# Kernel tuning notes

Measured on AMD Instinct MI355X. Metric: run time of the kernel, lower is better.

The kernel has to match this reference:

```python
import jax, jax.numpy as jnp
import numpy as np

NUM_BINS = 36
EPS = 1e-12
BASE_DROP, MIN_DROP, MAX_DROP = 0.3, 0.1, 0.6
SENSITIVITY, NORMAL_APE = 4.0, 0.78


def _hann(n):
    # torch.hann_window default (periodic=True): 0.5*(1 - cos(2*pi*k/N))
    return 0.5 - 0.5 * jnp.cos(2.0 * jnp.pi * jnp.arange(n, dtype=jnp.float32) / n)


def compute_ape(images):
    B, C, H, W = images.shape
    mean = jnp.array([0.485, 0.456, 0.406], dtype=images.dtype).reshape(1, 3, 1, 1)
    std = jnp.array([0.229, 0.224, 0.225], dtype=images.dtype).reshape(1, 3, 1, 1)
    wts = jnp.array([0.2989, 0.587, 0.114], dtype=images.dtype).reshape(1, 3, 1, 1)
    gray = ((images * std + mean) * wts).sum(axis=1)  # (B,H,W)
    gray = gray - gray.mean(axis=(1, 2), keepdims=True)
    gray = gray * (_hann(H)[:, None] * _hann(W)[None, :])
    P = jnp.abs(jnp.fft.fft2(gray)) ** 2
    P = jnp.fft.fftshift(P, axes=(1, 2))
    cy, cx = (H - 1) / 2.0, (W - 1) / 2.0
    yy = jnp.arange(H, dtype=jnp.float32)[:, None] - cy
    xx = jnp.arange(W, dtype=jnp.float32)[None, :] - cx
    r = jnp.sqrt(xx ** 2 + yy ** 2)
    theta = (jnp.arctan2(yy, xx) + 2 * jnp.pi) % (2 * jnp.pi)
    r_max = r.max()
    radial_mask = (r >= 0.05 * r_max) & (r <= 0.95 * r_max)
    bin_width = 2 * jnp.pi / NUM_BINS
    idx = jnp.clip((theta / bin_width).astype(jnp.int32), 0, NUM_BINS - 1)  # (H,W)
    # batched masked angular histogram: one segment_sum over B*NUM_BINS segments
    Pm = (P * radial_mask).reshape(B, -1)
    seg = (idx.reshape(-1)[None, :] + NUM_BINS * jnp.arange(B)[:, None]).reshape(-1)
    energy = jax.ops.segment_sum(Pm.reshape(-1), seg, num_segments=B * NUM_BINS)
    energy = energy.reshape(B, NUM_BINS)
    total = energy.sum(axis=1, keepdims=True)
    p = energy / (total + EPS)
    H_theta = -(p * jnp.log(p + EPS)).sum(axis=1)
    ape = jnp.clip(H_theta / np.log(NUM_BINS), 0.0, 1.0)
    return jnp.where(total[:, 0] <= EPS, 0.0, ape)


def ape_to_dropout_prob(ape):
    adj = jnp.tanh((NORMAL_APE - ape) * SENSITIVITY)
    drop = jnp.where(adj >= 0,
                     BASE_DROP + adj * (MAX_DROP - BASE_DROP),
                     BASE_DROP + adj * (BASE_DROP - MIN_DROP))
    return jnp.clip(drop, MIN_DROP, MAX_DROP)


def adaptive_dropout(x, probs, key):
    # per-sample dropout: mask ~ Bernoulli(1-p), scale by 1/(1-p+1e-8)
    p = probs[:, None, None]
    keep = jax.random.bernoulli(key, 1.0 - p, x.shape).astype(x.dtype)
    out = x * keep / (1.0 - p + 1e-8)
    return jnp.where(p > 0, out, x)


def setup_inputs() -> dict:
    key = jax.random.key(0)
    k1, k2, k3, k4 = jax.random.split(key, 4)
    B, N, D, Hf = 64, 256, 768, 768
    images = jax.random.uniform(k1, (B, 3, 448, 448), dtype=jnp.float32)
    x = jax.random.normal(k2, (B, N, D), dtype=jnp.float32)
    w1 = jax.random.normal(k3, (Hf, D), dtype=jnp.float32) * (1.0 / np.sqrt(D))
    w2 = jax.random.normal(k4, (D, Hf), dtype=jnp.float32) * (1.0 / np.sqrt(Hf))
    return {"images": images, "x": x, "w1": w1, "w2": w2}


def reference(images, x, w1, w2):
    ape = compute_ape(images)
    probs = jax.lax.stop_gradient(ape_to_dropout_prob(ape))  # torch casts to python float -> detached
    k0, k1, k2 = jax.random.split(jax.random.key(1), 3)
    h = adaptive_dropout(x, probs, k0)            # input dropout
    h = jnp.einsum('bnd,hd->bnh', h, w1)          # fc1 (bias=False)
    h = jax.nn.gelu(h, approximate=False)         # nn.GELU (exact erf)
    h = adaptive_dropout(h, probs, k1)
    y = jnp.einsum('bnh,dh->bnd', h, w2)          # fc2 (bias=False)
    y = adaptive_dropout(y, probs, k2)
    return y
```

## Files before the change

kernel.cpp:

```cpp
#include <hip/hip_runtime.h>
#include <stdint.h>
#include <math.h>

typedef __attribute__((ext_vector_type(8))) short short8;
typedef __attribute__((ext_vector_type(4))) float floatx4;

#define IMGN 448
#define HW   200704
#define NBATCH 64
#define NBINS 36

#define MFMA(a, b, c) __builtin_amdgcn_mfma_f32_16x16x32_bf16((a), (b), (c), 0, 0, 0)

#define WAITBAR6() asm volatile("s_waitcnt vmcnt(6)\ns_barrier" ::: "memory")
#define WAITBAR0() asm volatile("s_waitcnt vmcnt(0)\ns_barrier" ::: "memory")
#define ENDBAR()   asm volatile("s_waitcnt lgkmcnt(0)\ns_barrier" ::: "memory")

#define WS_WIN   0u
#define WS_BINS  4096u
#define WS_TS    24576u
#define WS_BIDX  32768u
#define WS_TW    1048576u
#define TWSZ     401408u
#define WS_W     4194304u
#define WSZ      1179648u
#define WS_REG1  16777216u
#define GSZ      25690112u
#define CBSZ     13762560u
#define XSZ      25165824u
#define WS_REG2  75497472u

__host__ __device__ __forceinline__ uint32_t rotl32(uint32_t v, int r) {
  return (v << r) | (v >> (32 - r));
}
__host__ __device__ __forceinline__ void tf2x32(uint32_t k0, uint32_t k1,
                                                uint32_t x0, uint32_t x1,
                                                uint32_t &o0, uint32_t &o1) {
  uint32_t k2 = k0 ^ k1 ^ 0x1BD11BDAu;
  uint32_t v0 = x0 + k0, v1 = x1 + k1;
#define TFR(r) { v0 += v1; v1 = rotl32(v1, r); v1 ^= v0; }
  TFR(13) TFR(15) TFR(26) TFR(6)   v0 += k1; v1 += k2 + 1u;
  TFR(17) TFR(29) TFR(16) TFR(24)  v0 += k2; v1 += k0 + 2u;
  TFR(13) TFR(15) TFR(26) TFR(6)   v0 += k0; v1 += k1 + 3u;
  TFR(17) TFR(29) TFR(16) TFR(24)  v0 += k1; v1 += k2 + 4u;
  TFR(13) TFR(15) TFR(26) TFR(6)   v0 += k2; v1 += k0 + 5u;
#undef TFR
  o0 = v0; o1 = v1;
}
__device__ __forceinline__ float tf_uniform(uint32_t k0, uint32_t k1, uint32_t idx) {
  uint32_t a, b;
  tf2x32(k0, k1, 0u, idx, a, b);
  uint32_t bits = a ^ b;
  return __uint_as_float((bits >> 9) | 0x3F800000u) - 1.0f;
}

__device__ __forceinline__ unsigned short bf16rne(float v) {
  unsigned u = __float_as_uint(v);
  return (unsigned short)((u + 0x7fffu + ((u >> 16) & 1u)) >> 16);
}
__device__ __forceinline__ void split2(float v, unsigned short &h, unsigned short &l) {
  h = bf16rne(v);
  float fh = __uint_as_float(((unsigned)h) << 16);
  l = bf16rne(v - fh);
}

__device__ __forceinline__ float fast_erf(float x) {
  float ax = fabsf(x);
  float t = 1.0f / (1.0f + 0.3275911f * ax);
  float p = t * (0.254829592f + t * (-0.284496736f + t * (1.421413741f +
            t * (-1.453152027f + t * 1.061405429f))));
  float y = 1.0f - p * __expf(-ax * ax);
  return __uint_as_float((__float_as_uint(y) & 0x7fffffffu) |
                         (__float_as_uint(x) & 0x80000000u));
}

__device__ __forceinline__ void gload16(const void *g, void *l) {
  __builtin_amdgcn_global_load_lds(
      (const __attribute__((address_space(1))) unsigned int *)g,
      (__attribute__((address_space(3))) unsigned int *)l, 16, 0, 0);
}

__global__ __launch_bounds__(256) void k_prep(float *__restrict__ win,
                                              double *__restrict__ bins,
                                              uint8_t *__restrict__ bidx) {
  int t = blockIdx.x * 256 + threadIdx.x;
  int a = t / IMGN, b = t % IMGN;
  double yy = (double)((a + 224) % IMGN) - 223.5;
  double xx = (double)((b + 224) % IMGN) - 223.5;
  double r2 = xx * xx + yy * yy;
  uint8_t idx = 255;
  if (r2 >= 249.76125 && r2 <= 90163.81125) {
    double th = atan2(yy, xx);
    if (th < 0.0) th += 6.283185307179586476925286766559;
    int i = (int)(th / 0.17453292519943295769236907684886);
    if (i > 35) i = 35;
    if (i < 0) i = 0;
    idx = (uint8_t)i;
  }
  bidx[t] = idx;
  if (t < IMGN) {
    double ang = 6.283185307179586476925286766559 * (double)t / 448.0;
    win[t] = (float)(0.5 - 0.5 * cos(ang));
  }
  if (t < NBATCH * NBINS) bins[t] = 0.0;
}

__global__ __launch_bounds__(256) void k_tw(short8 *__restrict__ tch, short8 *__restrict__ tcl,
                                            short8 *__restrict__ tsh, short8 *__restrict__ tsl) {
  int wid = blockIdx.x * 256 + threadIdx.x;
  int lane = wid & 63;
  int tmp = wid >> 6;
  int kb = tmp % 14, mb = tmp / 14;
  int m = mb * 16 + (lane & 15);
  int k0 = kb * 32 + (lane >> 4) * 8;
  short8 ch, cl, sh, sl;
#pragma unroll
  for (int e = 0; e < 8; ++e) {
    int mm = (m * (k0 + e)) % IMGN;
    double ang = -6.283185307179586476925286766559 * (double)mm / 448.0;
    float c = (float)cos(ang), s = (float)sin(ang);
    unsigned short h, l;
    split2(c, h, l); ch[e] = (short)h; cl[e] = (short)l;
    split2(s, h, l); sh[e] = (short)h; sl[e] = (short)l;
  }
  tch[wid] = ch; tcl[wid] = cl; tsh[wid] = sh; tsl[wid] = sl;
}

__global__ __launch_bounds__(256) void k_wconv(const float *__restrict__ w1, const float *__restrict__ w2,
                                               short8 *__restrict__ w1h, short8 *__restrict__ w1l,
                                               short8 *__restrict__ w2h, short8 *__restrict__ w2l) {
  int wid = blockIdx.x * 256 + threadIdx.x;
  const float *src = blockIdx.y ? w2 : w1;
  short8 *dh = blockIdx.y ? w2h : w1h;
  short8 *dl = blockIdx.y ? w2l : w1l;
  int lane = wid & 63;
  int tmp = wid >> 6;
  int kb = tmp % 24, nb = tmp / 24;
  int n = nb * 16 + (lane & 15);
  int k0 = kb * 32 + (lane >> 4) * 8;
  const float *p = src + (size_t)n * 768 + k0;
  short8 vh, vl;
#pragma unroll
  for (int e = 0; e < 8; ++e) {
    unsigned short h, l;
    split2(p[e], h, l);
    vh[e] = (short)h; vl[e] = (short)l;
  }
  dh[wid] = vh; dl[wid] = vl;
}

__global__ __launch_bounds__(256) void k_gprep(const float *__restrict__ img, const float *__restrict__ win,
                                               short8 *__restrict__ gh, short8 *__restrict__ gl) {
  int wid = blockIdx.x * 256 + threadIdx.x;
  int lane = wid & 63;
  int tmp = wid >> 6;
  int kb = tmp % 14, nb = tmp / 14;
  int n = nb * 16 + (lane & 15);
  int b = n / 448, y = n % 448;
  int x0 = kb * 32 + (lane >> 4) * 8;
  const float *p = img + (size_t)b * 3 * HW + y * IMGN + x0;
  float wy = win[y];
  short8 vh, vl;
#pragma unroll
  for (int e = 0; e < 8; ++e) {
    float r = p[e], g = p[HW + e], bl = p[2 * HW + e];
    float t0 = (r * 0.229f + 0.485f) * 0.2989f;
    float t1 = (g * 0.224f + 0.456f) * 0.587f;
    float t2 = (bl * 0.225f + 0.406f) * 0.114f;
    float v = ((t0 + t1) + t2) * wy * win[x0 + e];
    unsigned short h, l;
    split2(v, h, l);
    vh[e] = (short)h; vl[e] = (short)l;
  }
  gh[wid] = vh; gl[wid] = vl;
}

__global__ __launch_bounds__(256) void k_rows(const short8 *__restrict__ tch, const short8 *__restrict__ tcl,
                                              const short8 *__restrict__ tsh, const short8 *__restrict__ tsl,
                                              const short8 *__restrict__ gh, const short8 *__restrict__ gl,
                                              short8 *__restrict__ crh, short8 *__restrict__ crl,
                                              short8 *__restrict__ cih, short8 *__restrict__ cil) {
  __shared__ short8 S[512];
  int orig = blockIdx.x;
  int swz = (orig & 7) * 224 + (orig >> 3);
  int mtg = swz & 3, ntg = swz >> 2;
  int tid = threadIdx.x;
  int lane = tid & 63, w = tid >> 6;
  int g = lane >> 4, c = lane & 15;
  int mt = mtg * 4 + w;
  floatx4 s_c[4] = {}, s_s[4] = {};
  for (int kb = 0; kb < 14; ++kb) {
#pragma unroll
    for (int i = 0; i < 2; ++i) {
      int ch = w * 2 + i;
      const short8 *m0 = (ch >> 2) ? gl : gh;
      int row = ntg * 4 + (ch & 3);
      gload16(m0 + ((size_t)row * 14 + kb) * 64 + lane, (char *)S + ch * 1024);
    }
    int ao = (mt * 14 + kb) * 64 + lane;
    short8 ach = tch[ao], acl = tcl[ao], ash = tsh[ao], asl = tsl[ao];
    __syncthreads();
#pragma unroll
    for (int nt = 0; nt < 4; ++nt) {
      short8 bh = S[nt * 64 + lane];
      short8 bl = S[(4 + nt) * 64 + lane];
      s_c[nt] = MFMA(ach, bh, s_c[nt]);
      s_c[nt] = MFMA(ach, bl, s_c[nt]);
      s_c[nt] = MFMA(acl, bh, s_c[nt]);
      s_s[nt] = MFMA(ash, bh, s_s[nt]);
      s_s[nt] = MFMA(ash, bl, s_s[nt]);
      s_s[nt] = MFMA(asl, bh, s_s[nt]);
    }
    __syncthreads();
  }
#pragma unroll
  for (int nt = 0; nt < 4; ++nt) {
    int nrow = (ntg * 4 + nt) * 16 + c;
    int b = nrow / 448, y = nrow % 448;
    int kb2 = y >> 5;
    int lofs = 16 * ((y & 31) >> 3);
    int e2 = y & 7;
#pragma unroll
    for (int r = 0; r < 4; ++r) {
      int v = mt * 16 + 4 * g + r;
      if (v < 240) {
        int n2 = b * 240 + v;
        size_t word = ((size_t)(n2 >> 4) * 14 + kb2) * 64 + (n2 & 15) + lofs;
        unsigned short h, l;
        split2(s_c[nt][r], h, l);
        ((unsigned short *)crh)[word * 8 + e2] = h;
        ((unsigned short *)crl)[word * 8 + e2] = l;
        split2(s_s[nt][r], h, l);
        ((unsigned short *)cih)[word * 8 + e2] = h;
        ((unsigned short *)cil)[word * 8 + e2] = l;
      }
    }
  }
}

__global__ __launch_bounds__(128) void k_cols(const short8 *__restrict__ tch, const short8 *__restrict__ tcl,
                                              const short8 *__restrict__ tsh, const short8 *__restrict__ tsl,
                                              const short8 *__restrict__ crh, const short8 *__restrict__ crl,
                                              const short8 *__restrict__ cih, const short8 *__restrict__ cil,
                                              const uint8_t *__restrict__ bidx, double *__restrict__ bins) {
  __shared__ short8 S[1024];
  __shared__ double lb[72];
  int orig = blockIdx.x;
  int swz = (orig & 7) * 210 + (orig >> 3);
  int mtg = swz % 7, ntg = swz / 7;
  int tid = threadIdx.x;
  if (tid < 72) lb[tid] = 0.0;
  int lane = tid & 63, w = tid >> 6;
  int g = lane >> 4, c = lane & 15;
  int mt0 = mtg * 4 + w * 2;
  int nt0 = ntg * 4;
  floatx4 cc0[4] = {}, sc0[4] = {}, ss0[4] = {}, cs0[4] = {};
  floatx4 cc1[4] = {}, sc1[4] = {}, ss1[4] = {}, cs1[4] = {};
  for (int kb = 0; kb < 14; ++kb) {
#pragma unroll
    for (int i = 0; i < 8; ++i) {
      int ch = w * 8 + i;
      int sel = ch >> 2;
      const short8 *m0 = sel == 0 ? crh : sel == 1 ? crl : sel == 2 ? cih : cil;
      int row = nt0 + (ch & 3);
      gload16(m0 + ((size_t)row * 14 + kb) * 64 + lane, (char *)S + ch * 1024);
    }
    int ao = (mt0 * 14 + kb) * 64 + lane;
    short8 c0 = tch[ao], l0 = tcl[ao], s0 = tsh[ao], z0 = tsl[ao];
    short8 c1 = tch[ao + 896], l1 = tcl[ao + 896], s1 = tsh[ao + 896], z1 = tsl[ao + 896];
    __syncthreads();
#pragma unroll
    for (int nt = 0; nt < 4; ++nt) {
      short8 brh = S[nt * 64 + lane];
      short8 brl = S[(4 + nt) * 64 + lane];
      short8 bih = S[(8 + nt) * 64 + lane];
      short8 bil = S[(12 + nt) * 64 + lane];
      cc0[nt] = MFMA(c0, brh, cc0[nt]);
      cc0[nt] = MFMA(c0, brl, cc0[nt]);
      cc0[nt] = MFMA(l0, brh, cc0[nt]);
      sc0[nt] = MFMA(s0, brh, sc0[nt]);
      sc0[nt] = MFMA(s0, brl, sc0[nt]);
      sc0[nt] = MFMA(z0, brh, sc0[nt]);
      ss0[nt] = MFMA(s0, bih, ss0[nt]);
      ss0[nt] = MFMA(s0, bil, ss0[nt]);
      ss0[nt] = MFMA(z0, bih, ss0[nt]);
      cs0[nt] = MFMA(c0, bih, cs0[nt]);
      cs0[nt] = MFMA(c0, bil, cs0[nt]);
      cs0[nt] = MFMA(l0, bih, cs0[nt]);
      cc1[nt] = MFMA(c1, brh, cc1[nt]);
      cc1[nt] = MFMA(c1, brl, cc1[nt]);
      cc1[nt] = MFMA(l1, brh, cc1[nt]);
      sc1[nt] = MFMA(s1, brh, sc1[nt]);
      sc1[nt] = MFMA(s1, brl, sc1[nt]);
      sc1[nt] = MFMA(z1, brh, sc1[nt]);
      ss1[nt] = MFMA(s1, bih, ss1[nt]);
      ss1[nt] = MFMA(s1, bil, ss1[nt]);
      ss1[nt] = MFMA(z1, bih, ss1[nt]);
      cs1[nt] = MFMA(c1, bih, cs1[nt]);
      cs1[nt] = MFMA(c1, bil, cs1[nt]);
      cs1[nt] = MFMA(l1, bih, cs1[nt]);
    }
    __syncthreads();
  }
  int base_b = (ntg * 64) / 240;
  int cb0 = -1, cb1 = -1, cb2 = -1, cb3 = -1;
  double cv0 = 0.0, cv1 = 0.0, cv2 = 0.0, cv3 = 0.0;
#define PUTBIN(slot_, val_)                                                    \
  { int _s = (slot_); double _v = (val_);                                      \
    if (_s == cb0) cv0 += _v;                                                  \
    else if (_s == cb1) cv1 += _v;                                             \
    else if (_s == cb2) cv2 += _v;                                             \
    else if (_s == cb3) cv3 += _v;                                             \
    else {                                                                     \
      if (cb3 >= 0) atomicAdd(&lb[cb3], cv3);                                  \
      cb3 = cb2; cv3 = cv2; cb2 = cb1; cv2 = cv1;                              \
      cb1 = cb0; cv1 = cv0; cb0 = _s; cv0 = _v;                                \
    } }
#define C_EPI(CC, SC, SS, CS, MT)                                              \
  {                                                                            \
    _Pragma("unroll") for (int nt = 0; nt < 4; ++nt) {                         \
      int n = (nt0 + nt) * 16 + c;                                             \
      int v = n % 240;                                                         \
      int bloc = n / 240 - base_b;                                             \
      if (v < 225) {                                                           \
        _Pragma("unroll") for (int r = 0; r < 4; ++r) {                        \
          int u = (MT) * 16 + 4 * g + r;                                       \
          float frv = CC[nt][r] - SS[nt][r];                                   \
          float fiv = SC[nt][r] + CS[nt][r];                                   \
          double P = (double)frv * frv + (double)fiv * fiv;                    \
          int i1 = bidx[u * IMGN + v];                                         \
          if (i1 < 36) PUTBIN(bloc * 36 + i1, P);                              \
          if (v >= 1 && v <= 223) {                                            \
            int i2 = bidx[((IMGN - u) % IMGN) * IMGN + (IMGN - v)];            \
            if (i2 < 36) PUTBIN(bloc * 36 + i2, P);                            \
          }                                                                    \
        }                                                                      \
      }                                                                        \
    }                                                                          \
  }
  C_EPI(cc0, sc0, ss0, cs0, mt0)
  C_EPI(cc1, sc1, ss1, cs1, mt0 + 1)
#undef C_EPI
  if (cb0 >= 0) atomicAdd(&lb[cb0], cv0);
  if (cb1 >= 0) atomicAdd(&lb[cb1], cv1);
  if (cb2 >= 0) atomicAdd(&lb[cb2], cv2);
  if (cb3 >= 0) atomicAdd(&lb[cb3], cv3);
#undef PUTBIN
  __syncthreads();
  if (tid < 72) {
    int bb = base_b + tid / 36;
    if (bb < NBATCH && lb[tid] != 0.0) atomicAdd(&bins[bb * NBINS + (tid % 36)], lb[tid]);
  }
}

__global__ void k_probs(const double *__restrict__ bins, float *__restrict__ ts) {
  int b = threadIdx.x;
  if (b >= NBATCH) return;
  double T = 0.0;
  for (int i = 0; i < NBINS; ++i) T += bins[b * NBINS + i];
  double H = 0.0;
  for (int i = 0; i < NBINS; ++i) {
    double p = bins[b * NBINS + i] / (T + 1e-12);
    H -= p * log(p + 1e-12);
  }
  double ape = H / 3.5835189384561099;
  if (ape > 1.0) ape = 1.0;
  if (ape < 0.0) ape = 0.0;
  if (T <= 1e-12) ape = 0.0;
  double adj = tanh((0.78 - ape) * 4.0);
  double drop = (adj >= 0.0) ? (0.3 + adj * 0.3) : (0.3 + adj * 0.2);
  if (drop < 0.1) drop = 0.1;
  if (drop > 0.6) drop = 0.6;
  float p32 = (float)drop;
  ts[b] = 1.0f - p32;
  ts[NBATCH + b] = 1.0f / (1.0f - p32 + 1e-8f);
}

__global__ __launch_bounds__(256) void k_dropfrag(const float *__restrict__ x, const float *__restrict__ ts,
                                                  short8 *__restrict__ xh, short8 *__restrict__ xl,
                                                  uint32_t k0, uint32_t k1) {
  int wid = blockIdx.x * 256 + threadIdx.x;
  int lane = wid & 63;
  int tmp = wid >> 6;
  int kb = tmp % 24, mb = tmp / 24;
  int m = mb * 16 + (lane & 15);
  int d0 = kb * 32 + (lane >> 4) * 8;
  int bi = m >> 8;
  float t = ts[bi], s = ts[NBATCH + bi];
  const float *p = x + (size_t)m * 768 + d0;
  short8 vh, vl;
#pragma unroll
  for (int e = 0; e < 8; ++e) {
    uint32_t idx = (uint32_t)m * 768u + (uint32_t)(d0 + e);
    float u = tf_uniform(k0, k1, idx);
    float v = (u < t) ? p[e] * s : 0.0f;
    unsigned short h, l;
    split2(v, h, l);
    vh[e] = (short)h; vl[e] = (short)l;
  }
  xh[wid] = vh; xl[wid] = vl;
}

template <int MODE>
__global__ __launch_bounds__(256) void k_mlp(const short8 *__restrict__ ah, const short8 *__restrict__ al,
                                             const short8 *__restrict__ bh, const short8 *__restrict__ bl,
                                             const float *__restrict__ ts, float *__restrict__ out,
                                             short8 *__restrict__ oh, short8 *__restrict__ ol,
                                             uint32_t k0, uint32_t k1) {
  __shared__ short8 S[2][512];
  int orig = blockIdx.x;
  int swz = (orig & 7) * 192 + (orig >> 3);
  int ntg = swz % 12, mtg = swz / 12;
  int tid = threadIdx.x;
  int lane = tid & 63, w = tid >> 6;
  int g = lane >> 4, c = lane & 15;
  int mt0 = mtg * 8 + w * 2;
  int nt0 = ntg * 4;
  floatx4 acc0[4] = {}, acc1[4] = {};
  short8 aAh0, aAl0, aAh1, aAl1, aBh0, aBl0, aBh1, aBl1;

#define M_STAGE(buf, kb) { \
  _Pragma("unroll") for (int i = 0; i < 2; ++i) { \
    int ch = w * 2 + i; \
    const short8 *m0 = (ch >> 2) ? bl : bh; \
    int row = nt0 + (ch & 3); \
    gload16(m0 + ((size_t)row * 24 + (kb)) * 64 + lane, (char *)&S[buf][0] + ch * 1024); } }
#define M_LOADA(p, kb) { int ao = (mt0 * 24 + (kb)) * 64 + lane; \
  p##h0 = ah[ao]; p##l0 = al[ao]; \
  p##h1 = ah[ao + 24 * 64]; p##l1 = al[ao + 24 * 64]; }
#define M_COMPUTE(buf, p) { const short8 *Sc = &S[buf][0]; \
  _Pragma("unroll") for (int nt = 0; nt < 4; ++nt) { \
    short8 b_h = Sc[nt * 64 + lane]; \
    short8 b_l = Sc[(4 + nt) * 64 + lane]; \
    acc0[nt] = MFMA(p##h0, b_h, acc0[nt]); \
    acc0[nt] = MFMA(p##h0, b_l, acc0[nt]); \
    acc0[nt] = MFMA(p##l0, b_h, acc0[nt]); \
    acc1[nt] = MFMA(p##h1, b_h, acc1[nt]); \
    acc1[nt] = MFMA(p##h1, b_l, acc1[nt]); \
    acc1[nt] = MFMA(p##l1, b_h, acc1[nt]); } }

  M_STAGE(0, 0); M_LOADA(aA, 0);
  for (int kb = 0; kb < 24; kb += 2) {
    M_STAGE(1, kb + 1); M_LOADA(aB, kb + 1);
    WAITBAR6();
    M_COMPUTE(0, aA);
    ENDBAR();
    if (kb < 22) { M_STAGE(0, kb + 2); M_LOADA(aA, kb + 2); WAITBAR6(); }
    else { WAITBAR0(); }
    M_COMPUTE(1, aB);
    ENDBAR();
  }
#define M_EPI(ACC, MT)                                                         \
  {                                                                            \
    _Pragma("unroll") for (int nt = 0; nt < 4; ++nt) {                         \
      int n = (nt0 + nt) * 16 + c;                                             \
      _Pragma("unroll") for (int r = 0; r < 4; ++r) {                          \
        int m = (MT) * 16 + 4 * g + r;                                         \
        float val = ACC[nt][r];                                                \
        if (MODE == 1)                                                         \
          val = 0.5f * val * (1.0f + fast_erf(val * 0.70710678118654752440f)); \
        int bi = m >> 8;                                                       \
        float t = ts[bi], s = ts[NBATCH + bi];                                 \
        uint32_t idx = (uint32_t)m * 768u + (uint32_t)n;                       \
        float u = tf_uniform(k0, k1, idx);                                     \
        val = (u < t) ? val * s : 0.0f;                                        \
        if (MODE == 1) {                                                       \
          unsigned short hh, hl;                                               \
          split2(val, hh, hl);                                                 \
          int kb2 = n >> 5;                                                    \
          int lane2 = (m & 15) + 16 * ((n & 31) >> 3);                         \
          int e2 = n & 7;                                                      \
          size_t word = ((size_t)(m >> 4) * 24 + kb2) * 64 + lane2;            \
          ((unsigned short *)oh)[word * 8 + e2] = hh;                          \
          ((unsigned short *)ol)[word * 8 + e2] = hl;                          \
        } else {                                                               \
          out[(size_t)m * 768 + n] = val;                                      \
        }                                                                      \
      }                                                                        \
    }                                                                          \
  }
  M_EPI(acc0, mt0)
  M_EPI(acc1, mt0 + 1)
#undef M_EPI
}

extern "C" void kernel_launch(void *const *d_in, const int *in_sizes, int n_in,
                              void *d_out, int out_size, void *d_ws, size_t ws_size,
                              hipStream_t stream) {
  (void)in_sizes; (void)n_in; (void)out_size; (void)ws_size;
  const float *images = (const float *)d_in[0];
  const float *x  = (const float *)d_in[1];
  const float *w1 = (const float *)d_in[2];
  const float *w2 = (const float *)d_in[3];

  char *ws = (char *)d_ws;
  float   *win  = (float *)  (ws + WS_WIN);
  double  *bins = (double *) (ws + WS_BINS);
  float   *ts   = (float *)  (ws + WS_TS);
  uint8_t *bidx = (uint8_t *)(ws + WS_BIDX);
  short8  *tch  = (short8 *) (ws + WS_TW + 0 * TWSZ);
  short8  *tcl  = (short8 *) (ws + WS_TW + 1 * TWSZ);
  short8  *tsh  = (short8 *) (ws + WS_TW + 2 * TWSZ);
  short8  *tsl  = (short8 *) (ws + WS_TW + 3 * TWSZ);
  short8  *w1h  = (short8 *) (ws + WS_W + 0 * WSZ);
  short8  *w1l  = (short8 *) (ws + WS_W + 1 * WSZ);
  short8  *w2h  = (short8 *) (ws + WS_W + 2 * WSZ);
  short8  *w2l  = (short8 *) (ws + WS_W + 3 * WSZ);
  short8  *gh   = (short8 *) (ws + WS_REG1 + 0 * GSZ);
  short8  *gl   = (short8 *) (ws + WS_REG1 + 1 * GSZ);
  short8  *xh   = (short8 *) (ws + WS_REG1 + 0 * XSZ);
  short8  *xl   = (short8 *) (ws + WS_REG1 + 1 * XSZ);
  short8  *crh  = (short8 *) (ws + WS_REG2 + 0 * CBSZ);
  short8  *crl  = (short8 *) (ws + WS_REG2 + 1 * CBSZ);
  short8  *cih  = (short8 *) (ws + WS_REG2 + 2 * CBSZ);
  short8  *cil  = (short8 *) (ws + WS_REG2 + 3 * CBSZ);
  short8  *hh_  = (short8 *) (ws + WS_REG2 + 0 * XSZ);
  short8  *hl_  = (short8 *) (ws + WS_REG2 + 1 * XSZ);
  float   *yout = (float *)d_out;

  uint32_t keys[6];
  tf2x32(0u, 1u, 0u, 0u, keys[0], keys[1]);
  tf2x32(0u, 1u, 0u, 1u, keys[2], keys[3]);
  tf2x32(0u, 1u, 0u, 2u, keys[4], keys[5]);

  k_prep<<<784, 256, 0, stream>>>(win, bins, bidx);
  k_tw<<<98, 256, 0, stream>>>(tch, tcl, tsh, tsl);
  k_wconv<<<dim3(288, 2), 256, 0, stream>>>(w1, w2, w1h, w1l, w2h, w2l);
  k_gprep<<<6272, 256, 0, stream>>>(images, win, gh, gl);
  k_rows<<<1792, 256, 0, stream>>>(tch, tcl, tsh, tsl, gh, gl, crh, crl, cih, cil);
  k_cols<<<1680, 128, 0, stream>>>(tch, tcl, tsh, tsl, crh, crl, cih, cil, bidx, bins);
  k_probs<<<1, 64, 0, stream>>>(bins, ts);
  k_dropfrag<<<6144, 256, 0, stream>>>(x, ts, xh, xl, keys[0], keys[1]);
  k_mlp<1><<<1536, 256, 0, stream>>>(xh, xl, w1h, w1l, ts, yout, hh_, hl_, keys[2], keys[3]);
  k_mlp<2><<<1536, 256, 0, stream>>>(hh_, hl_, w2h, w2l, ts, yout, hh_, hl_, keys[4], keys[5]);
}
```

Measured before the change: 470.2 us.

## Retile row and column DFT GEMMs: more M-tiles per warp in rows, 4-warp cols

```diff
diff --git a/kernel.cpp b/kernel.cpp
--- a/kernel.cpp
+++ b/kernel.cpp
@@ -182,13 +182,13 @@
                                               short8 *__restrict__ cih, short8 *__restrict__ cil) {
   __shared__ short8 S[512];
   int orig = blockIdx.x;
-  int swz = (orig & 7) * 224 + (orig >> 3);
-  int mtg = swz & 3, ntg = swz >> 2;
+  int swz = (orig & 7) * 112 + (orig >> 3);
+  int mtg = swz & 1, ntg = swz >> 1;
   int tid = threadIdx.x;
   int lane = tid & 63, w = tid >> 6;
   int g = lane >> 4, c = lane & 15;
-  int mt = mtg * 4 + w;
-  floatx4 s_c[4] = {}, s_s[4] = {};
+  int mt0 = mtg * 8 + w * 2;
+  floatx4 sc0[4] = {}, ss0[4] = {}, sc1[4] = {}, ss1[4] = {};
   for (int kb = 0; kb < 14; ++kb) {
 #pragma unroll
     for (int i = 0; i < 2; ++i) {
@@ -197,48 +197,60 @@
       int row = ntg * 4 + (ch & 3);
       gload16(m0 + ((size_t)row * 14 + kb) * 64 + lane, (char *)S + ch * 1024);
     }
-    int ao = (mt * 14 + kb) * 64 + lane;
-    short8 ach = tch[ao], acl = tcl[ao], ash = tsh[ao], asl = tsl[ao];
+    int ao0 = (mt0 * 14 + kb) * 64 + lane;
+    int ao1 = ao0 + 14 * 64;
+    short8 c0 = tch[ao0], l0 = tcl[ao0], s0 = tsh[ao0], z0 = tsl[ao0];
+    short8 c1 = tch[ao1], l1 = tcl[ao1], s1 = tsh[ao1], z1 = tsl[ao1];
     __syncthreads();
 #pragma unroll
     for (int nt = 0; nt < 4; ++nt) {
       short8 bh = S[nt * 64 + lane];
       short8 bl = S[(4 + nt) * 64 + lane];
-      s_c[nt] = MFMA(ach, bh, s_c[nt]);
-      s_c[nt] = MFMA(ach, bl, s_c[nt]);
-      s_c[nt] = MFMA(acl, bh, s_c[nt]);
-      s_s[nt] = MFMA(ash, bh, s_s[nt]);
-      s_s[nt] = MFMA(ash, bl, s_s[nt]);
-      s_s[nt] = MFMA(asl, bh, s_s[nt]);
+      sc0[nt] = MFMA(c0, bh, sc0[nt]);
+      sc0[nt] = MFMA(c0, bl, sc0[nt]);
+      sc0[nt] = MFMA(l0, bh, sc0[nt]);
+      ss0[nt] = MFMA(s0, bh, ss0[nt]);
+      ss0[nt] = MFMA(s0, bl, ss0[nt]);
+      ss0[nt] = MFMA(z0, bh, ss0[nt]);
+      sc1[nt] = MFMA(c1, bh, sc1[nt]);
+      sc1[nt] = MFMA(c1, bl, sc1[nt]);
+      sc1[nt] = MFMA(l1, bh, sc1[nt]);
+      ss1[nt] = MFMA(s1, bh, ss1[nt]);
+      ss1[nt] = MFMA(s1, bl, ss1[nt]);
+      ss1[nt] = MFMA(z1, bh, ss1[nt]);
     }
     __syncthreads();
   }
-#pragma unroll
-  for (int nt = 0; nt < 4; ++nt) {
-    int nrow = (ntg * 4 + nt) * 16 + c;
-    int b = nrow / 448, y = nrow % 448;
-    int kb2 = y >> 5;
-    int lofs = 16 * ((y & 31) >> 3);
-    int e2 = y & 7;
-#pragma unroll
-    for (int r = 0; r < 4; ++r) {
-      int v = mt * 16 + 4 * g + r;
-      if (v < 240) {
-        int n2 = b * 240 + v;
-        size_t word = ((size_t)(n2 >> 4) * 14 + kb2) * 64 + (n2 & 15) + lofs;
-        unsigned short h, l;
-        split2(s_c[nt][r], h, l);
-        ((unsigned short *)crh)[word * 8 + e2] = h;
-        ((unsigned short *)crl)[word * 8 + e2] = l;
-        split2(s_s[nt][r], h, l);
-        ((unsigned short *)cih)[word * 8 + e2] = h;
-        ((unsigned short *)cil)[word * 8 + e2] = l;
-      }
-    }
-  }
-}
-
-__global__ __launch_bounds__(128) void k_cols(const short8 *__restrict__ tch, const short8 *__restrict__ tcl,
+#define R_EPI(SC, SS, MT)                                                      \
+  {                                                                            \
+    _Pragma("unroll") for (int nt = 0; nt < 4; ++nt) {                         \
+      int nrow = (ntg * 4 + nt) * 16 + c;                                      \
+      int b = nrow / 448, y = nrow % 448;                                      \
+      int kb2 = y >> 5;                                                        \
+      int lofs = 16 * ((y & 31) >> 3);                                         \
+      int e2 = y & 7;                                                          \
+      _Pragma("unroll") for (int r = 0; r < 4; ++r) {                          \
+        int v = (MT) * 16 + 4 * g + r;                                         \
+        if (v < 240) {                                                         \
+          int n2 = b * 240 + v;                                                \
+          size_t word = ((size_t)(n2 >> 4) * 14 + kb2) * 64 + (n2 & 15) + lofs;\
+          unsigned short h, l;                                                 \
+          split2(SC[nt][r], h, l);                                             \
+          ((unsigned short *)crh)[word * 8 + e2] = h;                          \
+          ((unsigned short *)crl)[word * 8 + e2] = l;                          \
+          split2(SS[nt][r], h, l);                                             \
+          ((unsigned short *)cih)[word * 8 + e2] = h;                          \
+          ((unsigned short *)cil)[word * 8 + e2] = l;                          \
+        }                                                                      \
+      }                                                                        \
+    }                                                                          \
+  }
+  R_EPI(sc0, ss0, mt0)
+  R_EPI(sc1, ss1, mt0 + 1)
+#undef R_EPI
+}
+
+__global__ __launch_bounds__(256) void k_cols(const short8 *__restrict__ tch, const short8 *__restrict__ tcl,
                                               const short8 *__restrict__ tsh, const short8 *__restrict__ tsl,
                                               const short8 *__restrict__ crh, const short8 *__restrict__ crl,
                                               const short8 *__restrict__ cih, const short8 *__restrict__ cil,
@@ -252,14 +264,16 @@
   if (tid < 72) lb[tid] = 0.0;
   int lane = tid & 63, w = tid >> 6;
   int g = lane >> 4, c = lane & 15;
-  int mt0 = mtg * 4 + w * 2;
+  int wm = w >> 1, wn = w & 1;
+  int mt0 = mtg * 4 + wm * 2;
+  int ntb = wn * 2;
   int nt0 = ntg * 4;
-  floatx4 cc0[4] = {}, sc0[4] = {}, ss0[4] = {}, cs0[4] = {};
-  floatx4 cc1[4] = {}, sc1[4] = {}, ss1[4] = {}, cs1[4] = {};
+  floatx4 cc0[2] = {}, sc0[2] = {}, ss0[2] = {}, cs0[2] = {};
+  floatx4 cc1[2] = {}, sc1[2] = {}, ss1[2] = {}, cs1[2] = {};
   for (int kb = 0; kb < 14; ++kb) {
 #pragma unroll
-    for (int i = 0; i < 8; ++i) {
-      int ch = w * 8 + i;
+    for (int i = 0; i < 4; ++i) {
+      int ch = w * 4 + i;
       int sel = ch >> 2;
       const short8 *m0 = sel == 0 ? crh : sel == 1 ? crl : sel == 2 ? cih : cil;
       int row = nt0 + (ch & 3);
@@ -270,11 +284,12 @@
     short8 c1 = tch[ao + 896], l1 = tcl[ao + 896], s1 = tsh[ao + 896], z1 = tsl[ao + 896];
     __syncthreads();
 #pragma unroll
-    for (int nt = 0; nt < 4; ++nt) {
-      short8 brh = S[nt * 64 + lane];
-      short8 brl = S[(4 + nt) * 64 + lane];
-      short8 bih = S[(8 + nt) * 64 + lane];
-      short8 bil = S[(12 + nt) * 64 + lane];
+    for (int nt = 0; nt < 2; ++nt) {
+      int ntl = ntb + nt;
+      short8 brh = S[ntl * 64 + lane];
+      short8 brl = S[(4 + ntl) * 64 + lane];
+      short8 bih = S[(8 + ntl) * 64 + lane];
+      short8 bil = S[(12 + ntl) * 64 + lane];
       cc0[nt] = MFMA(c0, brh, cc0[nt]);
       cc0[nt] = MFMA(c0, brl, cc0[nt]);
       cc0[nt] = MFMA(l0, brh, cc0[nt]);
@@ -318,8 +333,8 @@
     } }
 #define C_EPI(CC, SC, SS, CS, MT)                                              \
   {                                                                            \
-    _Pragma("unroll") for (int nt = 0; nt < 4; ++nt) {                         \
-      int n = (nt0 + nt) * 16 + c;                                             \
+    _Pragma("unroll") for (int nt = 0; nt < 2; ++nt) {                         \
+      int n = (nt0 + ntb + nt) * 16 + c;                                       \
       int v = n % 240;                                                         \
       int bloc = n / 240 - base_b;                                             \
       if (v < 225) {                                                           \
@@ -527,8 +542,8 @@
   k_tw<<<98, 256, 0, stream>>>(tch, tcl, tsh, tsl);
   k_wconv<<<dim3(288, 2), 256, 0, stream>>>(w1, w2, w1h, w1l, w2h, w2l);
   k_gprep<<<6272, 256, 0, stream>>>(images, win, gh, gl);
-  k_rows<<<1792, 256, 0, stream>>>(tch, tcl, tsh, tsl, gh, gl, crh, crl, cih, cil);
-  k_cols<<<1680, 128, 0, stream>>>(tch, tcl, tsh, tsl, crh, crl, cih, cil, bidx, bins);
+  k_rows<<<896, 256, 0, stream>>>(tch, tcl, tsh, tsl, gh, gl, crh, crl, cih, cil);
+  k_cols<<<1680, 256, 0, stream>>>(tch, tcl, tsh, tsl, crh, crl, cih, cil, bidx, bins);
   k_probs<<<1, 64, 0, stream>>>(bins, ts);
   k_dropfrag<<<6144, 256, 0, stream>>>(x, ts, xh, xl, keys[0], keys[1]);
   k_mlp<1><<<1536, 256, 0, stream>>>(xh, xl, w1h, w1l, ts, yout, hh_, hl_, keys[2], keys[3]);
```

Result: faster. 426.4 us (-9.3%).
